# Optimization experiments

Measured on AMD Instinct MI355X. Metric: run time of the kernel, lower is better.

Reference implementation:

```python
import jax, jax.numpy as jnp
import numpy as np

B, T, C = 2, 1024, 1024
H = 16
HD = C // H
S = 512   # short_term_memory_size
L = 1024  # sum(long_term_memory_size)
THETA = 10000.0


def setup_inputs() -> dict:
    key = jax.random.key(0)
    ks = jax.random.split(key, 7)
    return {
        "x": jax.random.normal(ks[0], (B, T, C), jnp.float32),
        "short_term_memory": jax.random.normal(ks[1], (B, S, C), jnp.float32),
        "long_q": jax.random.normal(ks[2], (B, L, H, HD), jnp.float32),
        "long_k": jax.random.normal(ks[3], (B, L, H, HD), jnp.float32),
        "long_v": jax.random.normal(ks[4], (B, L, H, HD), jnp.float32),
        "w_attn": jax.random.normal(ks[5], (C, 3 * C), jnp.float32) * 0.02,
        "w_proj": jax.random.normal(ks[6], (C, C), jnp.float32) * 0.02,
    }


def _rope_cos_sin(seq_len, dim, theta):
    # llama-style precompute_freqs_cis: freqs over even indices, angles = t * freq
    inv = 1.0 / (theta ** (jnp.arange(0, dim, 2, dtype=jnp.float32) / dim))
    t = jnp.arange(seq_len, dtype=jnp.float32)
    ang = jnp.outer(t, inv)  # [seq, dim//2]
    return jnp.cos(ang), jnp.sin(ang)


def _apply_rope(x, cos, sin):
    # x: [B, seq, H, hd] viewed as interleaved complex pairs (llama apply_rotary_emb)
    xr = x.reshape(*x.shape[:-1], HD // 2, 2)
    x0, x1 = xr[..., 0], xr[..., 1]
    c = cos[None, :, None, :]
    s = sin[None, :, None, :]
    o0 = x0 * c - x1 * s
    o1 = x0 * s + x1 * c
    return jnp.stack([o0, o1], axis=-1).reshape(x.shape)


def _memory_mask():
    # create_memory_mask: tril over M=L+S+T, rows [L, L+S) fully visible
    M = L + S + T
    m = np.tril(np.ones((M, M), dtype=np.float32))
    m[L:L + S, :] = 1.0
    return jnp.asarray(m)


_MASK = _memory_mask()


def reference(x, short_term_memory, long_q, long_k, long_v, w_attn, w_proj):
    # prepend short-term memory tokens, project qkv
    xcat = jnp.concatenate([short_term_memory, x], axis=1)          # [B, S+T, C]
    qkv = xcat @ w_attn                                             # [B, S+T, 3C]
    q, k, v = jnp.split(qkv, 3, axis=-1)
    q = q.reshape(B, S + T, H, HD)
    k = k.reshape(B, S + T, H, HD)
    v = v.reshape(B, S + T, H, HD)
    # in-place rotary on the last S+T positions (long-term part untouched)
    cos, sin = _rope_cos_sin(S + T, HD, THETA)
    q = _apply_rope(q, cos, sin)
    k = _apply_rope(k, cos, sin)
    # concat pre-rotated long-term memory in front
    q = jnp.concatenate([long_q, q], axis=1)                        # [B, M, H, hd]
    k = jnp.concatenate([long_k, k], axis=1)
    v = jnp.concatenate([long_v, v], axis=1)
    q, k, v = (t.transpose(0, 2, 1, 3) for t in (q, k, v))          # [B, H, M, hd]
    att = jnp.einsum('bhqd,bhkd->bhqk', q, k) * (1.0 / jnp.sqrt(jnp.float32(HD)))
    att = jnp.where(_MASK == 0, -jnp.inf, att)
    att = jax.nn.softmax(att, axis=-1)
    y = jnp.einsum('bhqk,bhkd->bhqd', att, v)                       # [B, H, M, hd]
    y = y.transpose(0, 2, 1, 3).reshape(B, L + S + T, C)
    y = y[:, -T:, :] @ w_proj                                       # [B, T, C]
    return y
```

## Files before the change

kernel.cpp:

```cpp
#include <hip/hip_runtime.h>
#include <math.h>

#define BB 2
#define TT 1024
#define CC 1024
#define HH 16
#define HD 64
#define SS 512
#define LL 1024
#define ST 1536
#define MM 2560
#define C3 3072

typedef __attribute__((ext_vector_type(8))) short short8;
typedef __attribute__((ext_vector_type(4))) short short4v;
typedef __attribute__((ext_vector_type(4))) float floatx4;

__device__ __forceinline__ unsigned short f2bf(float f) {
    union { float f; unsigned u; } v; v.f = f;
    unsigned r = v.u + 0x7fffu + ((v.u >> 16) & 1u);
    return (unsigned short)(r >> 16);
}
__device__ __forceinline__ float bf2f(short s) {
    union { unsigned u; float f; } v;
    v.u = ((unsigned)(unsigned short)s) << 16;
    return v.f;
}

__device__ __forceinline__ void gl_lds16(const short* g, short* l) {
    __builtin_amdgcn_global_load_lds(
        (const __attribute__((address_space(1))) void*)g,
        (__attribute__((address_space(3))) void*)l,
        16, 0, 0);
}

__global__ __launch_bounds__(256)
void prep_all(const float* __restrict__ x, const float* __restrict__ stm,
              const float* __restrict__ w_attn, const float* __restrict__ w_proj,
              const float* __restrict__ lk, const float* __restrict__ lv,
              short* __restrict__ Xb, short* __restrict__ WaT,
              short* __restrict__ WpT, short* __restrict__ Kg,
              short* __restrict__ Vt, float* __restrict__ tab)
{
    __shared__ __align__(16) char smem[9216];
    const int blk = blockIdx.x;
    const int t = threadIdx.x;

    if (blk < 3072) {
        const int idx = blk * 256 + t;
        const int rg  = idx >> 8;
        const int c   = (idx & 255) << 2;
        const int b   = rg >= ST;
        const int r   = rg - b * ST;
        const float* src = (r < SS) ? (stm + ((size_t)b * SS + r) * CC + c)
                                    : (x   + ((size_t)b * TT + (r - SS)) * CC + c);
        float4 v = *(const float4*)src;
        short4v o;
        o.x = (short)f2bf(v.x); o.y = (short)f2bf(v.y);
        o.z = (short)f2bf(v.z); o.w = (short)f2bf(v.w);
        *(short4v*)(Xb + (size_t)rg * CC + c) = o;
    } else if (blk < 7168) {
        const bool isA = blk < 6144;
        const int bx = isA ? (blk - 3072) : (blk - 6144);
        const int nblk = isA ? 96 : 32;
        const int Nd = isA ? C3 : CC;
        const float* W = isA ? w_attn : w_proj;
        short* WT = isA ? WaT : WpT;
        const int n0 = (bx % nblk) * 32, k0 = (bx / nblk) * 32;
        float (*Tl)[33] = (float(*)[33])smem;
        const int r = t >> 3, c4 = (t & 7) << 2;
        float4 v = *(const float4*)(W + (size_t)(k0 + r) * Nd + n0 + c4);
        Tl[r][c4 + 0] = v.x; Tl[r][c4 + 1] = v.y;
        Tl[r][c4 + 2] = v.z; Tl[r][c4 + 3] = v.w;
        __syncthreads();
        short4v o;
        o.x = (short)f2bf(Tl[c4 + 0][r]); o.y = (short)f2bf(Tl[c4 + 1][r]);
        o.z = (short)f2bf(Tl[c4 + 2][r]); o.w = (short)f2bf(Tl[c4 + 3][r]);
        *(short4v*)(WT + (size_t)(n0 + r) * CC + k0 + c4) = o;
    } else if (blk < 7360) {
        const int idx = (blk - 7168) * 256 + t;
        const int r = idx >> 5, e = idx & 31;
        const float inv = powf(10000.0f, -(float)e * (1.0f / 32.0f));
        float sn, cs;
        sincosf((float)r * inv, &sn, &cs);
        tab[idx * 2] = cs;
        tab[idx * 2 + 1] = sn;
    } else {
        const int bx = blk - 7360;
        const int bh = bx >> 4, j0 = (bx & 15) * 64;
        const int b = bh >> 4, h = bh & 15;
        short (*Tl)[72] = (short(*)[72])smem;
        const int jr = t >> 2, c16 = (t & 3) << 4;
        const size_t si = (((size_t)b * LL + j0 + jr) * HH + h) * HD + c16;
        short kk[16], vv[16];
        #pragma unroll
        for (int u = 0; u < 4; u++) {
            float4 kv = *(const float4*)(lk + si + 4 * u);
            float4 vf = *(const float4*)(lv + si + 4 * u);
            kk[4*u+0] = (short)f2bf(kv.x); kk[4*u+1] = (short)f2bf(kv.y);
            kk[4*u+2] = (short)f2bf(kv.z); kk[4*u+3] = (short)f2bf(kv.w);
            vv[4*u+0] = (short)f2bf(vf.x); vv[4*u+1] = (short)f2bf(vf.y);
            vv[4*u+2] = (short)f2bf(vf.z); vv[4*u+3] = (short)f2bf(vf.w);
        }
        short* kdst = Kg + ((size_t)bh * MM + j0 + jr) * HD + c16;
        *(short8*)kdst       = *(short8*)&kk[0];
        *(short8*)(kdst + 8) = *(short8*)&kk[8];
        #pragma unroll
        for (int u = 0; u < 16; u++) Tl[jr][c16 + u] = vv[u];
        __syncthreads();
        const int r = t >> 2, c = t & 3;
        short o0[8], o1[8];
        #pragma unroll
        for (int u = 0; u < 8; u++) {
            o0[u] = Tl[c * 16 + u][r];
            o1[u] = Tl[c * 16 + 8 + u][r];
        }
        short* vdst = Vt + ((size_t)bh * HD + r) * MM + j0 + c * 16;
        *(short8*)vdst       = *(short8*)&o0[0];
        *(short8*)(vdst + 8) = *(short8*)&o1[0];
    }
}

__global__ __launch_bounds__(256)
void qkv_gemm(const short* __restrict__ A, const short* __restrict__ Bt,
              const float* __restrict__ RT,
              short* __restrict__ Qo, short* __restrict__ Ko, short* __restrict__ Vo)
{
    __shared__ short As[128 * 32];
    __shared__ short Bs[128 * 32];
    __shared__ short Et[128 * 132];
    const int b = blockIdx.z;
    const int row0 = blockIdx.y * 128, col0 = blockIdx.x * 128;
    const int tid = threadIdx.x;
    const int w = tid >> 6, l = tid & 63, quad = l >> 4, cl = l & 15;
    const int wr = w >> 1, wc = w & 1;

    const int reg  = col0 >> 10;
    const bool hasQ = (row0 >= SS);
    if (reg == 0 && !hasQ) return;

    const int srow = (l >> 2);
    const int schunk = ((l & 3) - (srow >> 1)) & 3;
    const int arow = w * 32 + srow;
    const short* gA0 = A + ((size_t)b * ST + row0 + arow) * CC + schunk * 8;
    const short* gA1 = gA0 + (size_t)16 * CC;
    const short* gB0 = Bt + (size_t)(col0 + arow) * CC + schunk * 8;
    const short* gB1 = gB0 + (size_t)16 * CC;
    short* lA0 = &As[(w * 32) * 32 + l * 8];
    short* lA1 = &As[(w * 32 + 16) * 32 + l * 8];
    short* lB0 = &Bs[(w * 32) * 32 + l * 8];
    short* lB1 = &Bs[(w * 32 + 16) * 32 + l * 8];

    const int fs = (quad + (cl >> 1)) & 3;

    floatx4 acc[4][4];
    #pragma unroll
    for (int mi = 0; mi < 4; mi++)
        #pragma unroll
        for (int ni = 0; ni < 4; ni++) acc[mi][ni] = (floatx4){0.f, 0.f, 0.f, 0.f};

    for (int k0 = 0; k0 < CC; k0 += 32) {
        __syncthreads();
        gl_lds16(gA0 + k0, lA0);
        gl_lds16(gA1 + k0, lA1);
        gl_lds16(gB0 + k0, lB0);
        gl_lds16(gB1 + k0, lB1);
        __syncthreads();
        short8 af[4], bf[4];
        #pragma unroll
        for (int mi = 0; mi < 4; mi++)
            af[mi] = *(const short8*)&As[(wr * 64 + mi * 16 + cl) * 32 + fs * 8];
        #pragma unroll
        for (int ni = 0; ni < 4; ni++)
            bf[ni] = *(const short8*)&Bs[(wc * 64 + ni * 16 + cl) * 32 + fs * 8];
        #pragma unroll
        for (int mi = 0; mi < 4; mi++)
            #pragma unroll
            for (int ni = 0; ni < 4; ni++)
                acc[mi][ni] = __builtin_amdgcn_mfma_f32_16x16x32_bf16(
                    af[mi], bf[ni], acc[mi][ni], 0, 0, 0);
    }

    #pragma unroll
    for (int ni = 0; ni < 4; ni++) {
        const int c_local = wc * 64 + ni * 16 + cl;
        const int e = (c_local & 63) >> 1;
        #pragma unroll
        for (int mi = 0; mi < 4; mi++) {
            #pragma unroll
            for (int r = 0; r < 4; r++) {
                const int R_local = wr * 64 + mi * 16 + quad * 4 + r;
                const int R = row0 + R_local;
                float v = acc[mi][ni][r];
                if (reg < 2) {
                    const float2 tt = ((const float2*)RT)[R * 32 + e];
                    float po = __shfl_xor(v, 1);
                    float out = ((cl & 1) == 0) ? (v * tt.x - po * tt.y)
                                                : (po * tt.y + v * tt.x);
                    unsigned short bfv = f2bf(out);
                    int ob = __shfl_xor((int)bfv, 1);
                    if ((cl & 1) == 0) {
                        unsigned word = (unsigned)bfv | (((unsigned)ob & 0xffffu) << 16);
                        *(unsigned*)&Et[R_local * 132 + c_local] = word;
                    }
                } else {
                    Et[c_local * 132 + R_local] = (short)f2bf(v);
                }
            }
        }
    }
    __syncthreads();

    const int hh0 = (col0 & 1023) >> 6;
    if (reg < 2) {
        #pragma unroll
        for (int hf = 0; hf < 2; hf++) {
            const int hh = hh0 + hf;
            short* dstb = (reg == 0)
                ? Qo + (((size_t)b * HH + hh) * TT + (row0 - SS)) * HD
                : Ko + (((size_t)b * HH + hh) * MM + LL + row0) * HD;
            #pragma unroll
            for (int it = 0; it < 4; it++) {
                const int idx = it * 2048 + tid * 8;
                const int r = idx >> 6, d = idx & 63;
                short4v v0 = *(const short4v*)&Et[r * 132 + hf * 64 + d];
                short4v v1 = *(const short4v*)&Et[r * 132 + hf * 64 + d + 4];
                short8 vv;
                #pragma unroll
                for (int u = 0; u < 4; u++) { vv[u] = v0[u]; vv[u + 4] = v1[u]; }
                *(short8*)(dstb + idx) = vv;
            }
        }
    } else {
        #pragma unroll
        for (int it = 0; it < 8; it++) {
            const int idx = it * 2048 + tid * 8;
            const int c = idx >> 7, r0 = idx & 127;
            const int hh = hh0 + (c >> 6), d = c & 63;
            short4v v0 = *(const short4v*)&Et[c * 132 + r0];
            short4v v1 = *(const short4v*)&Et[c * 132 + r0 + 4];
            short8 vv;
            #pragma unroll
            for (int u = 0; u < 4; u++) { vv[u] = v0[u]; vv[u + 4] = v1[u]; }
            *(short8*)(Vo + (((size_t)b * HH + hh) * HD + d) * MM + LL + row0 + r0) = vv;
        }
    }
}

#define PSP 72
#define PSW (32 * PSP)
#define VS_OFF 4096
#define PS_OFF 8192
__global__ __launch_bounds__(256, 4)
void attn_mfma(const short* __restrict__ Qg, const short* __restrict__ Kg,
               const short* __restrict__ Vt, short* __restrict__ Op,
               float* __restrict__ Lp)
{
    __shared__ __align__(16) short L[17408];

    const int bh = blockIdx.x;
    const int q0 = (7 - blockIdx.y) * 128;
    const int piece = blockIdx.z;
    const int tid = threadIdx.x, w = tid >> 6, l = tid & 63;
    const int quad = l >> 4, cl = l & 15;

    short8 qa[2][2];
    #pragma unroll
    for (int g = 0; g < 2; g++) {
        const short* qptr = Qg + ((size_t)bh * TT + q0 + w * 32 + g * 16 + cl) * HD + quad * 8;
        qa[g][0] = *(const short8*)qptr;
        qa[g][1] = *(const short8*)(qptr + 32);
    }

    floatx4 o[2][4];
    float rs[2][4];
    #pragma unroll
    for (int g = 0; g < 2; g++)
        #pragma unroll
        for (int r = 0; r < 4; r++) {
            rs[g][r] = 0.f;
            o[g][r] = (floatx4){0.f, 0.f, 0.f, 0.f};
        }

    const int srow_lo = l >> 3;
    const int sslot  = l & 7;
    const int ch0 = (sslot - (srow_lo >> 1)) & 7;
    const int ch1 = (sslot - (4 + (srow_lo >> 1))) & 7;
    const int rowi0 = w * 16 + srow_lo;
    const int rowi1 = w * 16 + 8 + srow_lo;
    const short* kgb = Kg + (size_t)bh * MM * HD;
    const short* vbase = Vt + (size_t)bh * HD * MM;
    short* ldsK0 = &L[(w * 16) * 64];
    short* ldsK1 = &L[(w * 16 + 8) * 64];
    short* ldsV0 = &L[VS_OFF + (w * 16) * 64];
    short* ldsV1 = &L[VS_OFF + (w * 16 + 8) * 64];

    const int fsA = (quad + (cl >> 1)) & 7;
    const int fsB = (quad + 4 + (cl >> 1)) & 7;
    const int psA = (quad + 2 * cl) & 7;
    const int psB = (quad + 4 + 2 * cl) & 7;

    const int ntiles = (LL + SS + q0) / 64 + 2;
    const int t_begin = piece * ntiles / 4;
    const int t_end   = (piece + 1) * ntiles / 4;

    for (int t = t_begin; t < t_end; t++) {
        const int j0 = t * 64;
        __syncthreads();
        gl_lds16(kgb + (size_t)(j0 + rowi0) * HD + ch0 * 8, ldsK0);
        gl_lds16(kgb + (size_t)(j0 + rowi1) * HD + ch1 * 8, ldsK1);
        gl_lds16(vbase + (size_t)rowi0 * MM + j0 + ch0 * 8, ldsV0);
        gl_lds16(vbase + (size_t)rowi1 * MM + j0 + ch1 * 8, ldsV1);
        __syncthreads();

        floatx4 s[2][4];
        #pragma unroll
        for (int ks = 0; ks < 4; ks++) {
            const int krow = ks * 16 + cl;
            short8 kf0 = *(const short8*)&L[krow * 64 + fsA * 8];
            short8 kf1 = *(const short8*)&L[krow * 64 + fsB * 8];
            #pragma unroll
            for (int g = 0; g < 2; g++) {
                floatx4 z = (floatx4){0.f, 0.f, 0.f, 0.f};
                z = __builtin_amdgcn_mfma_f32_16x16x32_bf16(qa[g][0], kf0, z, 0, 0, 0);
                z = __builtin_amdgcn_mfma_f32_16x16x32_bf16(qa[g][1], kf1, z, 0, 0, 0);
                s[g][ks] = z;
            }
        }

        const bool tailzone = (t >= ntiles - 2);
        #pragma unroll
        for (int g = 0; g < 2; g++) {
            const int qgb = LL + SS + q0 + w * 32 + g * 16;
            #pragma unroll
            for (int ks = 0; ks < 4; ks++) {
                #pragma unroll
                for (int r = 0; r < 4; r++) {
                    float sv = s[g][ks][r] * 0.125f;
                    if (tailzone && (j0 + ks * 16 + cl > qgb + quad * 4 + r))
                        sv = -INFINITY;
                    const float p = __expf(sv);
                    rs[g][r] += p;
                    const int qrw = quad * 4 + r;
                    const int slot = (ks * 2 + (cl >> 3) + 2 * qrw) & 7;
                    L[PS_OFF + w * PSW + (g * 16 + qrw) * PSP + slot * 8 + (cl & 7)] =
                        (short)f2bf(p);
                }
            }
        }

        __builtin_amdgcn_s_waitcnt(0xc07f);
        __builtin_amdgcn_wave_barrier();

        short8 pf[2][2];
        #pragma unroll
        for (int g = 0; g < 2; g++) {
            pf[g][0] = *(const short8*)&L[PS_OFF + w * PSW + (g * 16 + cl) * PSP + psA * 8];
            pf[g][1] = *(const short8*)&L[PS_OFF + w * PSW + (g * 16 + cl) * PSP + psB * 8];
        }
        #pragma unroll
        for (int nt = 0; nt < 4; nt++) {
            const int drow = nt * 16 + cl;
            short8 vf0 = *(const short8*)&L[VS_OFF + drow * 64 + fsA * 8];
            short8 vf1 = *(const short8*)&L[VS_OFF + drow * 64 + fsB * 8];
            #pragma unroll
            for (int g = 0; g < 2; g++) {
                o[g][nt] = __builtin_amdgcn_mfma_f32_16x16x32_bf16(pf[g][0], vf0, o[g][nt], 0, 0, 0);
                o[g][nt] = __builtin_amdgcn_mfma_f32_16x16x32_bf16(pf[g][1], vf1, o[g][nt], 0, 0, 0);
            }
        }
    }

    #pragma unroll
    for (int g = 0; g < 2; g++)
        #pragma unroll
        for (int r = 0; r < 4; r++) {
            float t2 = rs[g][r];
            t2 += __shfl_xor(t2, 1);
            t2 += __shfl_xor(t2, 2);
            t2 += __shfl_xor(t2, 4);
            t2 += __shfl_xor(t2, 8);
            if (cl == 0)
                Lp[piece * 32768 + bh * 1024 + q0 + w * 32 + g * 16 + quad * 4 + r] = t2;
        }

    __syncthreads();
    #pragma unroll
    for (int g = 0; g < 2; g++)
        #pragma unroll
        for (int r = 0; r < 4; r++) {
            const int ql = w * 32 + g * 16 + quad * 4 + r;
            #pragma unroll
            for (int nt = 0; nt < 4; nt++)
                L[ql * 68 + nt * 16 + cl] = (short)f2bf(o[g][nt][r]);
        }
    __syncthreads();
    short* ob = Op + ((size_t)(piece * 32 + bh) * 1024 + q0) * 64;
    #pragma unroll
    for (int it = 0; it < 4; it++) {
        const int idx = it * 2048 + tid * 8;
        const int q = idx >> 6, d = idx & 63;
        short4v v0 = *(const short4v*)&L[q * 68 + d];
        short4v v1 = *(const short4v*)&L[q * 68 + d + 4];
        short8 vv;
        #pragma unroll
        for (int u = 0; u < 4; u++) { vv[u] = v0[u]; vv[u + 4] = v1[u]; }
        *(short8*)(ob + idx) = vv;
    }
}

__global__ __launch_bounds__(256)
void attn_combine(const short* __restrict__ Op, const float* __restrict__ Lp,
                  short* __restrict__ Yatt)
{
    const int idx = blockIdx.x * 256 + threadIdx.x;
    const int row = idx >> 3;
    const int seg = (idx & 7) << 3;
    const float lsum = Lp[row] + Lp[32768 + row] + Lp[65536 + row] + Lp[98304 + row];
    const float inv = 1.0f / lsum;
    float acc[8] = {0.f, 0.f, 0.f, 0.f, 0.f, 0.f, 0.f, 0.f};
    #pragma unroll
    for (int p = 0; p < 4; p++) {
        short8 v = *(const short8*)(Op + ((size_t)(p * 32768) + row) * 64 + seg);
        #pragma unroll
        for (int u = 0; u < 8; u++) acc[u] += bf2f(v[u]);
    }
    short8 o8;
    #pragma unroll
    for (int u = 0; u < 8; u++) o8[u] = (short)f2bf(acc[u] * inv);
    const int bh = row >> 10, q = row & 1023;
    const int b = bh >> 4, h = bh & 15;
    *(short8*)(Yatt + ((size_t)b * TT + q) * CC + h * 64 + seg) = o8;
}

__global__ __launch_bounds__(256)
void proj_gemm(const short* __restrict__ A, const short* __restrict__ Bt,
               float* __restrict__ Co)
{
    __shared__ short As[64 * 32];
    __shared__ short Bs[64 * 32];
    const int row0 = blockIdx.y * 64, col0 = blockIdx.x * 64;
    const int tid = threadIdx.x;
    const int w = tid >> 6, l = tid & 63, quad = l >> 4, cl = l & 15;
    const int wr = w >> 1, wc = w & 1;

    const int srow = tid >> 2;
    const int schunk = ((tid & 3) - ((srow & 15) >> 1)) & 3;
    const short* gA = A + (size_t)(row0 + srow) * CC + schunk * 8;
    const short* gB = Bt + (size_t)(col0 + srow) * CC + schunk * 8;
    short* lA = &As[tid * 8];
    short* lB = &Bs[tid * 8];

    const int fs = (quad + (cl >> 1)) & 3;

    floatx4 acc[2][2];
    #pragma unroll
    for (int mi = 0; mi < 2; mi++)
        #pragma unroll
        for (int ni = 0; ni < 2; ni++) acc[mi][ni] = (floatx4){0.f, 0.f, 0.f, 0.f};

    for (int k0 = 0; k0 < CC; k0 += 32) {
        __syncthreads();
        gl_lds16(gA + k0, lA);
        gl_lds16(gB + k0, lB);
        __syncthreads();
        short8 af[2], bf[2];
        #pragma unroll
        for (int mi = 0; mi < 2; mi++)
            af[mi] = *(const short8*)&As[(wr * 32 + mi * 16 + cl) * 32 + fs * 8];
        #pragma unroll
        for (int ni = 0; ni < 2; ni++)
            bf[ni] = *(const short8*)&Bs[(wc * 32 + ni * 16 + cl) * 32 + fs * 8];
        #pragma unroll
        for (int mi = 0; mi < 2; mi++)
            #pragma unroll
            for (int ni = 0; ni < 2; ni++)
                acc[mi][ni] = __builtin_amdgcn_mfma_f32_16x16x32_bf16(
                    af[mi], bf[ni], acc[mi][ni], 0, 0, 0);
    }
    #pragma unroll
    for (int mi = 0; mi < 2; mi++)
        #pragma unroll
        for (int ni = 0; ni < 2; ni++)
            #pragma unroll
            for (int r = 0; r < 4; r++)
                Co[(size_t)(row0 + wr * 32 + mi * 16 + quad * 4 + r) * CC
                   + col0 + wc * 32 + ni * 16 + cl] = acc[mi][ni][r];
}

extern "C" void kernel_launch(void* const* d_in, const int* in_sizes, int n_in,
                              void* d_out, int out_size, void* d_ws, size_t ws_size,
                              hipStream_t stream)
{
    (void)in_sizes; (void)n_in; (void)out_size; (void)ws_size;
    const float* x      = (const float*)d_in[0];
    const float* stm    = (const float*)d_in[1];
    const float* long_k = (const float*)d_in[3];
    const float* long_v = (const float*)d_in[4];
    const float* w_attn = (const float*)d_in[5];
    const float* w_proj = (const float*)d_in[6];
    float* out = (float*)d_out;

    short* Xb   = (short*)d_ws;
    short* WaT  = Xb   + (size_t)3145728;
    short* WpT  = WaT  + (size_t)3145728;
    short* Qb   = WpT  + (size_t)1048576;
    short* Kb   = Qb   + (size_t)2097152;
    short* Vtr  = Kb   + (size_t)5242880;
    short* Yb   = Vtr  + (size_t)5242880;
    float* RTab = (float*)(Yb + (size_t)2097152);
    short* Opart = (short*)(RTab + 98304);
    float* Lpart = (float*)(Opart + (size_t)8388608);

    prep_all<<<7872, 256, 0, stream>>>(x, stm, w_attn, w_proj, long_k, long_v,
                                       Xb, WaT, WpT, Kb, Vtr, RTab);

    qkv_gemm<<<dim3(24, 12, 2), 256, 0, stream>>>(Xb, WaT, RTab, Qb, Kb, Vtr);

    attn_mfma<<<dim3(32, 8, 4), 256, 0, stream>>>(Qb, Kb, Vtr, Opart, Lpart);
    attn_combine<<<1024, 256, 0, stream>>>(Opart, Lpart, Yb);

    proj_gemm<<<dim3(16, 32), 256, 0, stream>>>(Yb, WpT, out);
}
```

Measured before the change: 204.6 us.

## Fuse split-KV combine into projection GEMM and use exp2 with cheaper rounding

Removes the separate attn_combine kernel. proj_gemm now reads the four partial attention outputs and their row sums directly, normalizes them, and writes the bf16 A tile into LDS before each MFMA step. This drops a launch and the Yb round trip through memory. The cost is that each of the 16 column blocks re-reads and re-reduces the partials, which means 16x redundant combine traffic and extra work inside the GEMM loop. Separately, the softmax uses exp2 with a pre-scaled constant and a simpler round-half-up bf16 conversion for P.

```diff
diff --git a/kernel.cpp b/kernel.cpp
--- a/kernel.cpp
+++ b/kernel.cpp
@@ -21,11 +21,22 @@
     unsigned r = v.u + 0x7fffu + ((v.u >> 16) & 1u);
     return (unsigned short)(r >> 16);
 }
+__device__ __forceinline__ unsigned short p2bf(float f) {
+    union { float f; unsigned u; } v; v.f = f;
+    return (unsigned short)((v.u + 0x8000u) >> 16);
+}
 __device__ __forceinline__ float bf2f(short s) {
     union { unsigned u; float f; } v;
     v.u = ((unsigned)(unsigned short)s) << 16;
     return v.f;
 }
+
+#if __has_builtin(__builtin_amdgcn_exp2f)
+#define EXPP(x) __builtin_amdgcn_exp2f(x)
+#else
+#define EXPP(x) __expf((x) * 0.69314718056f)
+#endif
+#define SCL 0.18033688011112042f
 
 __device__ __forceinline__ void gl_lds16(const short* g, short* l) {
     __builtin_amdgcn_global_load_lds(
@@ -336,15 +347,15 @@
             for (int ks = 0; ks < 4; ks++) {
                 #pragma unroll
                 for (int r = 0; r < 4; r++) {
-                    float sv = s[g][ks][r] * 0.125f;
+                    float sv = s[g][ks][r] * SCL;
                     if (tailzone && (j0 + ks * 16 + cl > qgb + quad * 4 + r))
                         sv = -INFINITY;
-                    const float p = __expf(sv);
+                    const float p = EXPP(sv);
                     rs[g][r] += p;
                     const int qrw = quad * 4 + r;
                     const int slot = (ks * 2 + (cl >> 3) + 2 * qrw) & 7;
                     L[PS_OFF + w * PSW + (g * 16 + qrw) * PSP + slot * 8 + (cl & 7)] =
-                        (short)f2bf(p);
+                        (short)p2bf(p);
                 }
             }
         }
@@ -410,32 +421,8 @@
 }
 
 __global__ __launch_bounds__(256)
-void attn_combine(const short* __restrict__ Op, const float* __restrict__ Lp,
-                  short* __restrict__ Yatt)
-{
-    const int idx = blockIdx.x * 256 + threadIdx.x;
-    const int row = idx >> 3;
-    const int seg = (idx & 7) << 3;
-    const float lsum = Lp[row] + Lp[32768 + row] + Lp[65536 + row] + Lp[98304 + row];
-    const float inv = 1.0f / lsum;
-    float acc[8] = {0.f, 0.f, 0.f, 0.f, 0.f, 0.f, 0.f, 0.f};
-    #pragma unroll
-    for (int p = 0; p < 4; p++) {
-        short8 v = *(const short8*)(Op + ((size_t)(p * 32768) + row) * 64 + seg);
-        #pragma unroll
-        for (int u = 0; u < 8; u++) acc[u] += bf2f(v[u]);
-    }
-    short8 o8;
-    #pragma unroll
-    for (int u = 0; u < 8; u++) o8[u] = (short)f2bf(acc[u] * inv);
-    const int bh = row >> 10, q = row & 1023;
-    const int b = bh >> 4, h = bh & 15;
-    *(short8*)(Yatt + ((size_t)b * TT + q) * CC + h * 64 + seg) = o8;
-}
-
-__global__ __launch_bounds__(256)
-void proj_gemm(const short* __restrict__ A, const short* __restrict__ Bt,
-               float* __restrict__ Co)
+void proj_gemm(const short* __restrict__ Op, const float* __restrict__ Lp,
+               const short* __restrict__ Bt, float* __restrict__ Co)
 {
     __shared__ short As[64 * 32];
     __shared__ short Bs[64 * 32];
@@ -446,11 +433,15 @@
 
     const int srow = tid >> 2;
     const int schunk = ((tid & 3) - ((srow & 15) >> 1)) & 3;
-    const short* gA = A + (size_t)(row0 + srow) * CC + schunk * 8;
     const short* gB = Bt + (size_t)(col0 + srow) * CC + schunk * 8;
-    short* lA = &As[tid * 8];
     short* lB = &Bs[tid * 8];
 
+    const int ar = tid >> 2, ac = tid & 3;
+    const int aslot = (ac + ((ar & 15) >> 1)) & 3;
+    short* aw = &As[ar * 32 + aslot * 8];
+    const int b = row0 >> 10;
+    const int q = (row0 & 1023) + ar;
+
     const int fs = (quad + (cl >> 1)) & 3;
 
     floatx4 acc[2][2];
@@ -459,24 +450,43 @@
         #pragma unroll
         for (int ni = 0; ni < 2; ni++) acc[mi][ni] = (floatx4){0.f, 0.f, 0.f, 0.f};
 
-    for (int k0 = 0; k0 < CC; k0 += 32) {
-        __syncthreads();
-        gl_lds16(gA + k0, lA);
-        gl_lds16(gB + k0, lB);
-        __syncthreads();
-        short8 af[2], bf[2];
-        #pragma unroll
-        for (int mi = 0; mi < 2; mi++)
-            af[mi] = *(const short8*)&As[(wr * 32 + mi * 16 + cl) * 32 + fs * 8];
-        #pragma unroll
-        for (int ni = 0; ni < 2; ni++)
-            bf[ni] = *(const short8*)&Bs[(wc * 32 + ni * 16 + cl) * 32 + fs * 8];
-        #pragma unroll
-        for (int mi = 0; mi < 2; mi++)
+    for (int h = 0; h < HH; h++) {
+        const int lrow = (b * HH + h) * 1024 + q;
+        const float lsum = Lp[lrow] + Lp[32768 + lrow] + Lp[65536 + lrow] + Lp[98304 + lrow];
+        const float linv = 1.0f / lsum;
+        const short* opb = Op + ((size_t)(b * HH + h) * 1024 + q) * 64;
+        #pragma unroll
+        for (int kk = 0; kk < 2; kk++) {
+            const int k0 = h * 64 + kk * 32;
+            const int d0 = kk * 32 + ac * 8;
+            __syncthreads();
+            gl_lds16(gB + k0, lB);
+            float a8[8] = {0.f, 0.f, 0.f, 0.f, 0.f, 0.f, 0.f, 0.f};
+            #pragma unroll
+            for (int p = 0; p < 4; p++) {
+                short8 v = *(const short8*)(opb + (size_t)p * 2097152 + d0);
+                #pragma unroll
+                for (int u = 0; u < 8; u++) a8[u] += bf2f(v[u]);
+            }
+            short8 w8;
+            #pragma unroll
+            for (int u = 0; u < 8; u++) w8[u] = (short)f2bf(a8[u] * linv);
+            *(short8*)aw = w8;
+            __syncthreads();
+            short8 af[2], bf[2];
+            #pragma unroll
+            for (int mi = 0; mi < 2; mi++)
+                af[mi] = *(const short8*)&As[(wr * 32 + mi * 16 + cl) * 32 + fs * 8];
             #pragma unroll
             for (int ni = 0; ni < 2; ni++)
-                acc[mi][ni] = __builtin_amdgcn_mfma_f32_16x16x32_bf16(
-                    af[mi], bf[ni], acc[mi][ni], 0, 0, 0);
+                bf[ni] = *(const short8*)&Bs[(wc * 32 + ni * 16 + cl) * 32 + fs * 8];
+            #pragma unroll
+            for (int mi = 0; mi < 2; mi++)
+                #pragma unroll
+                for (int ni = 0; ni < 2; ni++)
+                    acc[mi][ni] = __builtin_amdgcn_mfma_f32_16x16x32_bf16(
+                        af[mi], bf[ni], acc[mi][ni], 0, 0, 0);
+        }
     }
     #pragma unroll
     for (int mi = 0; mi < 2; mi++)
@@ -518,7 +528,6 @@
     qkv_gemm<<<dim3(24, 12, 2), 256, 0, stream>>>(Xb, WaT, RTab, Qb, Kb, Vtr);
 
     attn_mfma<<<dim3(32, 8, 4), 256, 0, stream>>>(Qb, Kb, Vtr, Opart, Lpart);
-    attn_combine<<<1024, 256, 0, stream>>>(Opart, Lpart, Yb);
-
-    proj_gemm<<<dim3(16, 32), 256, 0, stream>>>(Yb, WpT, out);
-}
+
+    proj_gemm<<<dim3(16, 32), 256, 0, stream>>>(Opart, Lpart, WpT, out);
+}
```

New measurement: 214.1 us. 4.6% more time.
